# Performance work log

Hardware: AMD Instinct MI355X
Metric: run time of the kernel (lower is better)

## Reference

```python
import jax, jax.numpy as jnp
import numpy as np

IN_FEATURES = 512
DIM_EXPLOSION = 20
OUT_FEATURES = IN_FEATURES * DIM_EXPLOSION  # 10240
NB_PROJ_ENTRIES = 6
HASH_LENGTH = 32
BATCH = 4096


def _make_sparse_proj(key):
    """Sparse binary random projection: each of the OUT_FEATURES rows has
    NB_PROJ_ENTRIES entries set to 1 (as in OlfactoryModel.create_rand_proj_matrix)."""
    idx = jax.random.randint(key, (OUT_FEATURES, NB_PROJ_ENTRIES), 0, IN_FEATURES)
    rows = jnp.arange(OUT_FEATURES)[:, None]
    W = jnp.zeros((OUT_FEATURES, IN_FEATURES), dtype=jnp.float32)
    return W.at[rows, idx].set(1.0)


def setup_inputs() -> dict:
    key = jax.random.key(0)
    k1, k2 = jax.random.split(key)
    inp = jax.random.uniform(k1, (BATCH, IN_FEATURES), dtype=jnp.float32)
    W = _make_sparse_proj(k2)
    return {"input": inp, "weight": W, "hash_length": HASH_LENGTH}


def reference(input, weight, hash_length):
    # F.linear: [B, in] @ [out, in]^T -> [B, out]
    x = jnp.einsum('bi,oi->bo', input, weight)
    # MB_sparsify: winner-take-all, keep top `hash_length` activations per row, zero the rest
    topv = jax.lax.top_k(x, hash_length)[0]          # [B, k]
    thresh = topv[:, -1:]                            # k-th largest per row
    return jnp.where(x >= thresh, x, jnp.zeros_like(x))
```

## Files before the change

### kernel.cpp

```cpp
#include <hip/hip_runtime.h>


constexpr int IN_F   = 512;
constexpr int OUT_F  = 10240;
constexpr int TPB    = 512;
constexpr int VPT    = OUT_F / TPB;
constexpr int NBINS  = 2048;
constexpr int NCHUNK = NBINS / 4;
constexpr int NWAVES = TPB / 64;

static_assert(NCHUNK == TPB, "chunk scan assumes one chunk per thread");

__global__ __launch_bounds__(256) void extract_idx(const float* __restrict__ W,
                                                   uint4* __restrict__ packed,
                                                   int out_f) {
  int row  = blockIdx.x * 4 + (threadIdx.x >> 6);
  int lane = threadIdx.x & 63;
  if (row >= out_f) return;

  const float* wr = W + (size_t)row * IN_F;
  unsigned long long masks[8];
#pragma unroll
  for (int c = 0; c < 8; ++c) {
    float v = wr[c * 64 + lane];
    masks[c] = __ballot(v != 0.0f);
  }
  if (lane == 0) {
    unsigned idx[6] = {IN_F, IN_F, IN_F, IN_F, IN_F, IN_F};
    int n = 0;
#pragma unroll
    for (int c = 0; c < 8; ++c) {
      unsigned long long m = masks[c];
      while (m && n < 6) {
        int b = __builtin_ctzll(m);
        idx[n++] = (unsigned)(c * 64 + b);
        m &= m - 1;
      }
    }
    uint4 r;
    r.x = idx[0] | (idx[1] << 16);
    r.y = idx[2] | (idx[3] << 16);
    r.z = idx[4] | (idx[5] << 16);
    r.w = (unsigned)n;
    packed[row] = r;
  }
}

__global__ __launch_bounds__(TPB) void fly_hash(const float* __restrict__ inp,
                                                const uint4* __restrict__ packed,
                                                const int* __restrict__ kptr,
                                                float* __restrict__ out) {
  __shared__ float inRow[IN_F + 1];
  __shared__ int   hist[NBINS];
  __shared__ int   csum[NCHUNK];
  __shared__ int   wsum[NWAVES];
  __shared__ unsigned sh_bstar;

  const int tid = threadIdx.x;
  const int row = blockIdx.x;
  const int k   = *kptr;

  if (tid < IN_F) inRow[tid] = inp[(size_t)row * IN_F + tid];
  if (tid == 0)   inRow[IN_F] = 0.0f;
  for (int i = tid; i < NBINS; i += TPB) hist[i] = 0;
  __syncthreads();

  float x[VPT];
#pragma unroll
  for (int i = 0; i < VPT; ++i) {
    uint4 r = packed[tid + i * TPB];
    float s = inRow[r.x & 0xFFFFu];
    s += inRow[r.x >> 16];
    s += inRow[r.y & 0xFFFFu];
    s += inRow[r.y >> 16];
    s += inRow[r.z & 0xFFFFu];
    s += inRow[r.z >> 16];
    x[i] = s;
    int bin = (int)(s * 256.0f);
    bin = bin < 0 ? 0 : (bin > NBINS - 1 ? NBINS - 1 : bin);
    atomicAdd(&hist[bin], 1);
  }
  __syncthreads();

  {
    int b0 = tid * 4;
    csum[tid] = hist[b0] + hist[b0 + 1] + hist[b0 + 2] + hist[b0 + 3];
  }
  __syncthreads();
  for (int s = 1; s < NCHUNK; s <<= 1) {
    int v = csum[tid] + ((tid + s < NCHUNK) ? csum[tid + s] : 0);
    __syncthreads();
    csum[tid] = v;
    __syncthreads();
  }
  {
    int above = (tid + 1 < NCHUNK) ? csum[tid + 1] : 0;
    if (csum[tid] >= k && above < k) {
      int acc = above;
      unsigned bsel = (unsigned)(tid * 4);
      for (int b = tid * 4 + 3; b >= tid * 4; --b) {
        acc += hist[b];
        if (acc >= k) { bsel = (unsigned)b; break; }
      }
      sh_bstar = bsel;
    }
  }
  __syncthreads();

  const unsigned bstar = sh_bstar;
  unsigned lo = __float_as_uint((float)bstar * (1.0f / 256.0f));
  lo = (lo >= 8u) ? lo - 8u : 0u;
  unsigned hi = __float_as_uint((float)(bstar + 1) * (1.0f / 256.0f)) + 8u;

  const int lane = tid & 63;
  const int wid  = tid >> 6;
  while (lo < hi) {
    unsigned mid = lo + ((hi - lo + 1u) >> 1);
    float fm = __uint_as_float(mid);
    int c = 0;
#pragma unroll
    for (int i = 0; i < VPT; ++i)
      c += (int)__popcll(__ballot(x[i] >= fm));
    if (lane == 0) wsum[wid] = c;
    __syncthreads();
    int total = 0;
#pragma unroll
    for (int w = 0; w < NWAVES; ++w) total += wsum[w];
    if (total >= k) lo = mid; else hi = mid - 1;
    __syncthreads();
  }
  const float t = __uint_as_float(lo);

  float* orow = out + (size_t)row * OUT_F;
#pragma unroll
  for (int i = 0; i < VPT; ++i) {
    float v = x[i];
    orow[tid + i * TPB] = (v >= t) ? v : 0.0f;
  }
}

extern "C" void kernel_launch(void* const* d_in, const int* in_sizes, int n_in,
                              void* d_out, int out_size, void* d_ws, size_t ws_size,
                              hipStream_t stream) {
  const float* inp = (const float*)d_in[0];
  const float* W   = (const float*)d_in[1];
  const int* kptr  = (const int*)d_in[2];
  float* out       = (float*)d_out;

  const int batch = in_sizes[0] / IN_F;
  const int out_f = in_sizes[1] / IN_F;

  uint4* packed = (uint4*)d_ws;

  hipLaunchKernelGGL(extract_idx, dim3((out_f + 3) / 4), dim3(256), 0, stream,
                     W, packed, out_f);
  hipLaunchKernelGGL(fly_hash, dim3(batch), dim3(TPB), 0, stream,
                     inp, packed, kptr, out);
}
```

Baseline: 256.9 us.

## Process four batch rows per block with interleaved float4 input and narrowed histogram

```diff
diff --git a/kernel.cpp b/kernel.cpp
--- a/kernel.cpp
+++ b/kernel.cpp
@@ -1,15 +1,19 @@
 #include <hip/hip_runtime.h>
 
+
+typedef float f4 __attribute__((ext_vector_type(4)));
 
 constexpr int IN_F   = 512;
 constexpr int OUT_F  = 10240;
 constexpr int TPB    = 512;
-constexpr int VPT    = OUT_F / TPB;
-constexpr int NBINS  = 2048;
-constexpr int NCHUNK = NBINS / 4;
+constexpr int ROWS   = 4;
+constexpr int FPT    = OUT_F / TPB;
+constexpr int NBINS  = 1024;
+constexpr int CHUNK  = 8;
+constexpr int NCHUNK = NBINS / CHUNK;
 constexpr int NWAVES = TPB / 64;
 
-static_assert(NCHUNK == TPB, "chunk scan assumes one chunk per thread");
+static_assert(ROWS * NCHUNK == TPB, "scan assumes one chunk per thread");
 
 __global__ __launch_bounds__(256) void extract_idx(const float* __restrict__ W,
                                                    uint4* __restrict__ packed,
@@ -46,96 +50,149 @@
   }
 }
 
-__global__ __launch_bounds__(TPB) void fly_hash(const float* __restrict__ inp,
-                                                const uint4* __restrict__ packed,
-                                                const int* __restrict__ kptr,
-                                                float* __restrict__ out) {
-  __shared__ float inRow[IN_F + 1];
-  __shared__ int   hist[NBINS];
-  __shared__ int   csum[NCHUNK];
-  __shared__ int   wsum[NWAVES];
-  __shared__ unsigned sh_bstar;
-
-  const int tid = threadIdx.x;
-  const int row = blockIdx.x;
-  const int k   = *kptr;
-
-  if (tid < IN_F) inRow[tid] = inp[(size_t)row * IN_F + tid];
-  if (tid == 0)   inRow[IN_F] = 0.0f;
-  for (int i = tid; i < NBINS; i += TPB) hist[i] = 0;
+__global__ __launch_bounds__(TPB, 4) void fly_hash(const float* __restrict__ inp,
+                                                   const uint4* __restrict__ packed,
+                                                   const int* __restrict__ kptr,
+                                                   float* __restrict__ out) {
+  __shared__ f4  in4[IN_F + 1];
+  __shared__ int hist[ROWS * NBINS];
+  __shared__ int csum[TPB];
+  __shared__ int wsum[NWAVES][ROWS];
+  __shared__ int sh_bstar[ROWS];
+
+  const int tid  = threadIdx.x;
+  const int row0 = blockIdx.x * ROWS;
+  const int k    = *kptr;
+
+  {
+    const float* p = inp + (size_t)row0 * IN_F + tid;
+    f4 v;
+    v.x = p[0];
+    v.y = p[IN_F];
+    v.z = p[2 * IN_F];
+    v.w = p[3 * IN_F];
+    in4[tid] = v;
+  }
+  if (tid == 0) { f4 z = {0.0f, 0.0f, 0.0f, 0.0f}; in4[IN_F] = z; }
+  if (tid < ROWS) sh_bstar[tid] = -1;
+  for (int i = tid; i < ROWS * NBINS; i += TPB) hist[i] = 0;
   __syncthreads();
 
-  float x[VPT];
-#pragma unroll
-  for (int i = 0; i < VPT; ++i) {
+  f4 x4[FPT];
+#pragma unroll
+  for (int i = 0; i < FPT; ++i) {
     uint4 r = packed[tid + i * TPB];
-    float s = inRow[r.x & 0xFFFFu];
-    s += inRow[r.x >> 16];
-    s += inRow[r.y & 0xFFFFu];
-    s += inRow[r.y >> 16];
-    s += inRow[r.z & 0xFFFFu];
-    s += inRow[r.z >> 16];
-    x[i] = s;
-    int bin = (int)(s * 256.0f);
-    bin = bin < 0 ? 0 : (bin > NBINS - 1 ? NBINS - 1 : bin);
-    atomicAdd(&hist[bin], 1);
+    f4 s = in4[r.x & 0xFFFFu];
+    s += in4[r.x >> 16];
+    s += in4[r.y & 0xFFFFu];
+    s += in4[r.y >> 16];
+    s += in4[r.z & 0xFFFFu];
+    s += in4[r.z >> 16];
+    x4[i] = s;
+#pragma unroll
+    for (int r2 = 0; r2 < ROWS; ++r2) {
+      float v = (r2 == 0) ? s.x : (r2 == 1) ? s.y : (r2 == 2) ? s.z : s.w;
+      if (v >= 4.0f) {
+        int b = (int)((v - 4.0f) * 512.0f);
+        b = b > NBINS - 1 ? NBINS - 1 : b;
+        atomicAdd(&hist[r2 * NBINS + b], 1);
+      }
+    }
   }
   __syncthreads();
 
   {
-    int b0 = tid * 4;
-    csum[tid] = hist[b0] + hist[b0 + 1] + hist[b0 + 2] + hist[b0 + 3];
-  }
-  __syncthreads();
-  for (int s = 1; s < NCHUNK; s <<= 1) {
-    int v = csum[tid] + ((tid + s < NCHUNK) ? csum[tid + s] : 0);
+    const int r = tid >> 7;
+    const int c = tid & (NCHUNK - 1);
+    const int base = r * NBINS + c * CHUNK;
+    int ssum = 0;
+#pragma unroll
+    for (int j = 0; j < CHUNK; ++j) ssum += hist[base + j];
+    csum[tid] = ssum;
     __syncthreads();
-    csum[tid] = v;
-    __syncthreads();
-  }
-  {
-    int above = (tid + 1 < NCHUNK) ? csum[tid + 1] : 0;
+    for (int st = 1; st < NCHUNK; st <<= 1) {
+      int v = csum[tid] + ((c + st < NCHUNK) ? csum[tid + st] : 0);
+      __syncthreads();
+      csum[tid] = v;
+      __syncthreads();
+    }
+    int above = (c + 1 < NCHUNK) ? csum[tid + 1] : 0;
     if (csum[tid] >= k && above < k) {
       int acc = above;
-      unsigned bsel = (unsigned)(tid * 4);
-      for (int b = tid * 4 + 3; b >= tid * 4; --b) {
-        acc += hist[b];
-        if (acc >= k) { bsel = (unsigned)b; break; }
-      }
-      sh_bstar = bsel;
+      int bsel = c * CHUNK;
+      for (int b = c * CHUNK + CHUNK - 1; b >= c * CHUNK; --b) {
+        acc += hist[r * NBINS + b];
+        if (acc >= k) { bsel = b; break; }
+      }
+      sh_bstar[r] = bsel;
     }
   }
   __syncthreads();
 
-  const unsigned bstar = sh_bstar;
-  unsigned lo = __float_as_uint((float)bstar * (1.0f / 256.0f));
-  lo = (lo >= 8u) ? lo - 8u : 0u;
-  unsigned hi = __float_as_uint((float)(bstar + 1) * (1.0f / 256.0f)) + 8u;
-
+  unsigned lo[ROWS], hi[ROWS];
+#pragma unroll
+  for (int r = 0; r < ROWS; ++r) {
+    int b = sh_bstar[r];
+    if (b < 0) {
+      lo[r] = 0u;
+      hi[r] = __float_as_uint(4.0f + (1.0f / 512.0f));
+    } else {
+      lo[r] = __float_as_uint(4.0f + (float)b * (1.0f / 512.0f));
+      hi[r] = __float_as_uint(4.0f + (float)(b + 1) * (1.0f / 512.0f));
+    }
+  }
   const int lane = tid & 63;
   const int wid  = tid >> 6;
-  while (lo < hi) {
-    unsigned mid = lo + ((hi - lo + 1u) >> 1);
-    float fm = __uint_as_float(mid);
-    int c = 0;
-#pragma unroll
-    for (int i = 0; i < VPT; ++i)
-      c += (int)__popcll(__ballot(x[i] >= fm));
-    if (lane == 0) wsum[wid] = c;
+  while (lo[0] < hi[0] || lo[1] < hi[1] || lo[2] < hi[2] || lo[3] < hi[3]) {
+    unsigned mid[ROWS];
+    float fm[ROWS];
+#pragma unroll
+    for (int r = 0; r < ROWS; ++r) {
+      mid[r] = lo[r] + ((hi[r] - lo[r] + 1u) >> 1);
+      fm[r] = __uint_as_float(mid[r]);
+    }
+    int c0 = 0, c1 = 0, c2 = 0, c3 = 0;
+#pragma unroll
+    for (int i = 0; i < FPT; ++i) {
+      c0 += (int)__popcll(__ballot(x4[i].x >= fm[0]));
+      c1 += (int)__popcll(__ballot(x4[i].y >= fm[1]));
+      c2 += (int)__popcll(__ballot(x4[i].z >= fm[2]));
+      c3 += (int)__popcll(__ballot(x4[i].w >= fm[3]));
+    }
+    if (lane == 0) {
+      wsum[wid][0] = c0; wsum[wid][1] = c1; wsum[wid][2] = c2; wsum[wid][3] = c3;
+    }
     __syncthreads();
-    int total = 0;
-#pragma unroll
-    for (int w = 0; w < NWAVES; ++w) total += wsum[w];
-    if (total >= k) lo = mid; else hi = mid - 1;
+    int tot[ROWS] = {0, 0, 0, 0};
+#pragma unroll
+    for (int w = 0; w < NWAVES; ++w)
+#pragma unroll
+      for (int r = 0; r < ROWS; ++r) tot[r] += wsum[w][r];
+#pragma unroll
+    for (int r = 0; r < ROWS; ++r) {
+      if (lo[r] < hi[r]) {
+        if (tot[r] >= k) lo[r] = mid[r]; else hi[r] = mid[r] - 1u;
+      }
+    }
     __syncthreads();
   }
-  const float t = __uint_as_float(lo);
-
-  float* orow = out + (size_t)row * OUT_F;
-#pragma unroll
-  for (int i = 0; i < VPT; ++i) {
-    float v = x[i];
-    orow[tid + i * TPB] = (v >= t) ? v : 0.0f;
+  const float t0 = __uint_as_float(lo[0]);
+  const float t1 = __uint_as_float(lo[1]);
+  const float t2 = __uint_as_float(lo[2]);
+  const float t3 = __uint_as_float(lo[3]);
+
+  float* o0 = out + (size_t)(row0 + 0) * OUT_F;
+  float* o1 = out + (size_t)(row0 + 1) * OUT_F;
+  float* o2 = out + (size_t)(row0 + 2) * OUT_F;
+  float* o3 = out + (size_t)(row0 + 3) * OUT_F;
+#pragma unroll
+  for (int i = 0; i < FPT; ++i) {
+    int f = tid + i * TPB;
+    f4 v = x4[i];
+    o0[f] = (v.x >= t0) ? v.x : 0.0f;
+    o1[f] = (v.y >= t1) ? v.y : 0.0f;
+    o2[f] = (v.z >= t2) ? v.z : 0.0f;
+    o3[f] = (v.w >= t3) ? v.w : 0.0f;
   }
 }
 
@@ -154,6 +211,6 @@
 
   hipLaunchKernelGGL(extract_idx, dim3((out_f + 3) / 4), dim3(256), 0, stream,
                      W, packed, out_f);
-  hipLaunchKernelGGL(fly_hash, dim3(batch), dim3(TPB), 0, stream,
+  hipLaunchKernelGGL(fly_hash, dim3(batch / ROWS), dim3(TPB), 0, stream,
                      inp, packed, kptr, out);
 }
```

Measured after the change: 283.0 us. 1.1x slower.
